# Kernel optimization log

Measured on AMD Instinct MI355X. Metric: run time of the kernel, lower is better.

## Reference

```python
import jax, jax.numpy as jnp
from jax import lax
import numpy as np

B, H, W = 8, 256, 256
NH = 128          # num_hiddens
NRH = 32          # num_residual_hiddens
K = 1024          # num_embeddings
D = 128           # embedding_dim
CC = 0.25         # commitment_cost


def setup_inputs() -> dict:
    key = jax.random.key(0)
    ks = jax.random.split(key, 18)

    def w(k, shape):
        fan_in = int(np.prod(shape[1:]))
        return (jax.random.normal(k, shape, jnp.float32) / np.sqrt(fan_in)).astype(jnp.float32)

    inp = {
        "x": jax.random.normal(ks[0], (B, 3, H, W), jnp.float32),
        # encoder
        "enc_c1": w(ks[1], (NH // 2, 3, 4, 4)),        # conv4x4 s2
        "enc_c2": w(ks[2], (NH, NH // 2, 4, 4)),       # conv4x4 s2
        "enc_c3": w(ks[3], (NH, NH, 3, 3)),            # conv3x3
        "enc_r1a": w(ks[4], (NRH, NH, 3, 3)),
        "enc_r1b": w(ks[5], (NH, NRH, 1, 1)),
        "enc_r2a": w(ks[6], (NRH, NH, 3, 3)),
        "enc_r2b": w(ks[7], (NH, NRH, 1, 1)),
        "pre_vq_w": w(ks[8], (D, NH, 1, 1)),
        # codebook: uniform(-1/K, 1/K) as in original init
        "codebook": jax.random.uniform(ks[9], (K, D), jnp.float32, -1.0 / K, 1.0 / K),
        # decoder
        "dec_c1": w(ks[10], (NH, D, 3, 3)),
        "dec_r1a": w(ks[11], (NRH, NH, 3, 3)),
        "dec_r1b": w(ks[12], (NH, NRH, 1, 1)),
        "dec_r2a": w(ks[13], (NRH, NH, 3, 3)),
        "dec_r2b": w(ks[14], (NH, NRH, 1, 1)),
        # ConvTranspose2d weight, torch layout [Cin, Cout, 4, 4]
        "dec_dc": w(ks[15], (NH, NH // 2, 4, 4)),
        "dec_c3": w(ks[16], (3, NH // 2, 3, 3)),
    }
    return inp


def _conv(x, w, s, p):
    return lax.conv_general_dilated(x, w, (s, s), ((p, p), (p, p)),
                                    dimension_numbers=("NCHW", "OIHW", "NCHW"))


def _deconv4x4_s2_p1(x, w_t):
    # torch ConvTranspose2d(k=4, s=2, p=1): flip kernel, swap in/out, lhs-dilate
    w = jnp.transpose(w_t[:, :, ::-1, ::-1], (1, 0, 2, 3))  # [Cout, Cin, 4, 4]
    return lax.conv_general_dilated(x, w, (1, 1), ((2, 2), (2, 2)),
                                    lhs_dilation=(2, 2),
                                    dimension_numbers=("NCHW", "OIHW", "NCHW"))


def _res_stack(x, r1a, r1b, r2a, r2b):
    for a, b in ((r1a, r1b), (r2a, r2b)):
        h = _conv(jax.nn.relu(x), a, 1, 1)
        h = _conv(jax.nn.relu(h), b, 1, 0)
        x = x + h
    return jax.nn.relu(x)


def _resize1d_align(x, axis, out_size):
    n = x.shape[axis]
    pos = jnp.arange(out_size, dtype=jnp.float32) * ((n - 1) / (out_size - 1))
    lo = jnp.floor(pos).astype(jnp.int32)
    hi = jnp.minimum(lo + 1, n - 1)
    wt = (pos - lo.astype(jnp.float32)).astype(x.dtype)
    shape = [1] * x.ndim
    shape[axis] = out_size
    wt = wt.reshape(shape)
    return jnp.take(x, lo, axis=axis) * (1 - wt) + jnp.take(x, hi, axis=axis) * wt


def _upsample2x_bilinear_align(x):  # align_corners=True, separable
    x = _resize1d_align(x, 2, 2 * x.shape[2])
    return _resize1d_align(x, 3, 2 * x.shape[3])


def reference(x, enc_c1, enc_c2, enc_c3, enc_r1a, enc_r1b, enc_r2a, enc_r2b,
              pre_vq_w, codebook, dec_c1, dec_r1a, dec_r1b, dec_r2a, dec_r2b,
              dec_dc, dec_c3):
    # ---- encoder ----
    h = jax.nn.relu(_conv(x, enc_c1, 2, 1))
    h = jax.nn.relu(_conv(h, enc_c2, 2, 1))
    h = _conv(h, enc_c3, 1, 1)            # note: no relu here (matches source)
    h = _res_stack(h, enc_r1a, enc_r1b, enc_r2a, enc_r2b)
    z = _conv(h, pre_vq_w, 1, 0)          # [B, D, H/4, W/4]

    # ---- VQ (eval mode: no EMA update, q_latent_loss = 0) ----
    zp = jnp.transpose(z, (0, 2, 3, 1))               # [B, h, w, D]
    flat = zp.reshape(-1, D)                          # [N, D]
    dist = (jnp.sum(flat * flat, axis=1, keepdims=True)
            + jnp.sum(codebook * codebook, axis=1)
            - 2.0 * flat @ codebook.T)                # [N, K]
    idx = jnp.argmin(dist, axis=1)                    # [N]
    q = codebook[idx].reshape(zp.shape)               # gather lookup
    e_latent_loss = jnp.mean((lax.stop_gradient(q) - zp) ** 2)
    loss = CC * e_latent_loss
    q_st = zp + lax.stop_gradient(q - zp)             # straight-through
    counts = jnp.zeros((K,), jnp.float32).at[idx].add(1.0)
    avg_probs = counts / flat.shape[0]
    perplexity = jnp.exp(-jnp.sum(avg_probs * jnp.log(avg_probs + 1e-10)))
    quantized = jnp.transpose(q_st, (0, 3, 1, 2))     # [B, D, h, w]

    # ---- decoder ----
    d = _conv(quantized, dec_c1, 1, 1)
    d = _res_stack(d, dec_r1a, dec_r1b, dec_r2a, dec_r2b)
    d = jax.nn.relu(_deconv4x4_s2_p1(d, dec_dc))
    d = _upsample2x_bilinear_align(d)
    d = _conv(d, dec_c3, 1, 1)
    recon = 2.0 * jax.nn.sigmoid(d) - 1.0             # [B, 3, H, W]
    return loss, recon, perplexity
```

## Files before the change

kernel.cpp:

```cpp
#include <hip/hip_runtime.h>
#include <hip/hip_bf16.h>
#include <math.h>

#define CC_COST 0.25

typedef __attribute__((ext_vector_type(8))) short short8v;
typedef __attribute__((ext_vector_type(4))) float f32x4;
typedef __attribute__((ext_vector_type(16))) float f32x16;

__device__ __forceinline__ unsigned short f2bf(float f) {
    unsigned u = __float_as_uint(f);
    unsigned r = (u + 0x7FFFu + ((u >> 16) & 1u)) >> 16;
    return (unsigned short)r;
}
__device__ __forceinline__ float bf2f(unsigned short h) {
    return __uint_as_float(((unsigned)h) << 16);
}


struct WtJobs {
    const float* src[15];
    float* dst[15];
    int cout[15], cin[15], kk[15], kind[15];
    int blk0[16];
};

__global__ void wt_batch_k(WtJobs J)
{
    int blk = blockIdx.x;
    int j = 0;
    while (j < 14 && blk >= J.blk0[j + 1]) ++j;
    int i = (blk - J.blk0[j]) * 256 + threadIdx.x;
    int total = J.cout[j] * J.cin[j] * J.kk[j];
    if (i >= total) return;
    const float* src = J.src[j];
    float* dst = J.dst[j];
    int kind = J.kind[j];
    if (kind == 0) {
        int Cout = J.cout[j], Cin = J.cin[j], KK = J.kk[j];
        int oc = i % Cout; int t2 = i / Cout; int t = t2 % KK; int c = t2 / KK;
        dst[i] = src[(oc * Cin + c) * KK + t];
    } else {
        int o = i % 3; int t = (i / 3) % 9; int c = i / 27;
        dst[i] = src[(o * 64 + c) * 9 + t];
    }
}

__global__ void wt_split_k(const float* __restrict__ w,
                           unsigned short* __restrict__ whi,
                           unsigned short* __restrict__ wlo)
{
    int i = blockIdx.x * 256 + threadIdx.x;
    if (i >= 147456) return;
    int ci = i & 15;
    int oc = (i >> 4) & 127;
    int rest = i >> 11;
    int cb = rest & 7;
    int tap = rest >> 3;
    float v = w[(oc * 128 + cb * 16 + ci) * 9 + tap];
    unsigned short h = f2bf(v);
    whi[i] = h;
    wlo[i] = f2bf(v - bf2f(h));
}

__global__ void wt_split4_k(const float* __restrict__ w,
                            unsigned short* __restrict__ whi,
                            unsigned short* __restrict__ wlo)
{
    int i = blockIdx.x * 256 + threadIdx.x;
    if (i >= 131072) return;
    int t = i & 15;
    int oc = (i >> 4) & 127;
    int rest = i >> 11;
    int cb = rest & 3;
    int tap = rest >> 2;
    float v = w[(oc * 64 + cb * 16 + t) * 16 + tap];
    unsigned short h = f2bf(v);
    whi[i] = h;
    wlo[i] = f2bf(v - bf2f(h));
}

__global__ void wt_split_dc_k(const float* __restrict__ w,
                              unsigned short* __restrict__ whi,
                              unsigned short* __restrict__ wlo)
{
    int i = blockIdx.x * 256 + threadIdx.x;
    if (i >= 131072) return;
    int ci = i & 15;
    int oc = (i >> 4) & 63;
    int cb = (i >> 10) & 7;
    int kx = (i >> 13) & 3;
    int ky = i >> 15;
    float v = w[((size_t)(cb * 16 + ci) * 64 + oc) * 16 + ky * 4 + kx];
    unsigned short h = f2bf(v);
    whi[i] = h;
    wlo[i] = f2bf(v - bf2f(h));
}

__global__ void wt_split_r_k(const float* __restrict__ w,
                             unsigned short* __restrict__ whi,
                             unsigned short* __restrict__ wlo)
{
    int i = blockIdx.x * 256 + threadIdx.x;
    if (i >= 36864) return;
    int k5 = i & 31;
    int oc = (i >> 5) & 31;
    int cb = (i >> 10) & 3;
    int tap = i >> 12;
    float v = w[(oc * 128 + cb * 32 + k5) * 9 + tap];
    unsigned short h = f2bf(v);
    whi[i] = h;
    wlo[i] = f2bf(v - bf2f(h));
}

__global__ void wt_split_1x1_k(const float* __restrict__ w,
                               unsigned short* __restrict__ whi,
                               unsigned short* __restrict__ wlo)
{
    int i = blockIdx.x * 256 + threadIdx.x;
    if (i >= 4096) return;
    int ci = i & 15;
    int oc = (i >> 4) & 127;
    int kk = i >> 11;
    float v = w[oc * 32 + kk * 16 + ci];
    unsigned short h = f2bf(v);
    whi[i] = h;
    wlo[i] = f2bf(v - bf2f(h));
}

__global__ void wt_split_up_k(const float* __restrict__ w,
                              unsigned short* __restrict__ whi,
                              unsigned short* __restrict__ wlo)
{
    int i = blockIdx.x * 256 + threadIdx.x;
    if (i >= 18432) return;
    int ci = i & 15;
    int oc = (i >> 4) & 31;
    int cb = (i >> 9) & 3;
    int tap = i >> 11;
    float v = 0.f;
    if (oc < 3) {
        int ch = cb * 16 + ci;
        v = w[(oc * 64 + ch) * 9 + tap];
    }
    unsigned short h = f2bf(v);
    whi[i] = h;
    wlo[i] = f2bf(v - bf2f(h));
}

__global__ __launch_bounds__(512) void conv3x3_mfma(
    const float* __restrict__ in,
    const unsigned short* __restrict__ whi,
    const unsigned short* __restrict__ wlo,
    float* __restrict__ out)
{
    constexpr int CST = 40;
    __shared__ unsigned short ls_hi[4 * 68 * CST];
    __shared__ unsigned short ls_lo[4 * 68 * CST];

    int tid = threadIdx.x;
    int lane = tid & 63;
    int w = tid >> 6;
    int myrow = w & 1;
    int oc0 = (w >> 1) * 32;
    int y0 = (blockIdx.x & 31) * 2;
    int b  = blockIdx.x >> 5;
    int ln31 = lane & 31;
    int lhf  = lane >> 5;

    f32x16 acc0 = {};
    f32x16 acc1 = {};

    const float* inb = in + (size_t)b * 128 * 4096;

    for (int chunk = 0; chunk < 4; ++chunk) {
        int c0 = chunk * 32;
        __syncthreads();
        for (int i = tid; i < 4 * 66 * 16; i += 512) {
            int x = i % 66;
            int t = i / 66;
            int cp = t & 15;
            int r = t >> 4;
            int gy = y0 - 1 + r, gx = x - 1;
            float v0 = 0.f, v1 = 0.f;
            if ((unsigned)gy < 64u && (unsigned)gx < 64u) {
                const float* p = inb + (size_t)(c0 + 2 * cp) * 4096 + gy * 64 + gx;
                v0 = p[0];
                v1 = p[4096];
            }
            unsigned short h0 = f2bf(v0), h1 = f2bf(v1);
            unsigned short l0 = f2bf(v0 - bf2f(h0)), l1 = f2bf(v1 - bf2f(h1));
            int a = (r * 68 + x) * CST + 2 * cp;
            *reinterpret_cast<unsigned int*>(&ls_hi[a]) = (unsigned)h0 | ((unsigned)h1 << 16);
            *reinterpret_cast<unsigned int*>(&ls_lo[a]) = (unsigned)l0 | ((unsigned)l1 << 16);
        }
        __syncthreads();

        #pragma unroll
        for (int tap = 0; tap < 9; ++tap) {
            int dy = tap / 3, dx = tap - 3 * (tap / 3);
            int rbase = (myrow + dy) * 68;
            #pragma unroll
            for (int cb = 0; cb < 2; ++cb) {
                int cbg = chunk * 2 + cb;
                size_t wofs = (((size_t)tap * 8 + cbg) * 128 + oc0 + ln31) * 16 + lhf * 8;
                short8v ah = *reinterpret_cast<const short8v*>(whi + wofs);
                short8v al = *reinterpret_cast<const short8v*>(wlo + wofs);
                int k0 = cb * 16 + lhf * 8;
                int xo0 = (rbase + ln31 + dx) * CST + k0;
                int xo1 = (rbase + 32 + ln31 + dx) * CST + k0;
                short8v bh0 = *reinterpret_cast<const short8v*>(&ls_hi[xo0]);
                short8v bl0 = *reinterpret_cast<const short8v*>(&ls_lo[xo0]);
                short8v bh1 = *reinterpret_cast<const short8v*>(&ls_hi[xo1]);
                short8v bl1 = *reinterpret_cast<const short8v*>(&ls_lo[xo1]);
                acc0 = __builtin_amdgcn_mfma_f32_32x32x16_bf16(ah, bh0, acc0, 0, 0, 0);
                acc1 = __builtin_amdgcn_mfma_f32_32x32x16_bf16(ah, bh1, acc1, 0, 0, 0);
                acc0 = __builtin_amdgcn_mfma_f32_32x32x16_bf16(ah, bl0, acc0, 0, 0, 0);
                acc1 = __builtin_amdgcn_mfma_f32_32x32x16_bf16(ah, bl1, acc1, 0, 0, 0);
                acc0 = __builtin_amdgcn_mfma_f32_32x32x16_bf16(al, bh0, acc0, 0, 0, 0);
                acc1 = __builtin_amdgcn_mfma_f32_32x32x16_bf16(al, bh1, acc1, 0, 0, 0);
            }
        }
    }

    float* ob = out + (size_t)b * 128 * 4096 + (size_t)(y0 + myrow) * 64;
    #pragma unroll
    for (int r = 0; r < 16; ++r) {
        int oc = oc0 + (r & 3) + 8 * (r >> 2) + 4 * lhf;
        ob[(size_t)oc * 4096 + ln31]      = acc0[r];
        ob[(size_t)oc * 4096 + 32 + ln31] = acc1[r];
    }
}

__global__ __launch_bounds__(512) void conv4x4s2_mfma(
    const float* __restrict__ in,
    const unsigned short* __restrict__ whi,
    const unsigned short* __restrict__ wlo,
    float* __restrict__ out)
{
    constexpr int CST = 24;
    __shared__ unsigned short lsEh[6 * 65 * CST];
    __shared__ unsigned short lsEl[6 * 65 * CST];
    __shared__ unsigned short lsOh[6 * 65 * CST];
    __shared__ unsigned short lsOl[6 * 65 * CST];

    int tid = threadIdx.x;
    int lane = tid & 63;
    int w = tid >> 6;
    int myrow = w & 1;
    int oc0 = (w >> 1) * 32;
    int y0 = (blockIdx.x & 31) * 2;
    int b  = blockIdx.x >> 5;
    int ln31 = lane & 31;
    int lhf  = lane >> 5;

    f32x16 acc0 = {};
    f32x16 acc1 = {};

    const float* inb = in + (size_t)b * 64 * 16384;

    for (int cb = 0; cb < 4; ++cb) {
        int c0 = cb * 16;
        __syncthreads();
        for (int i = tid; i < 12480; i += 512) {
            int gxi = i % 130; int t2 = i / 130;
            int r = t2 % 6; int cc = t2 / 6;
            int gx = gxi - 1;
            int gy = 2 * y0 - 1 + r;
            float v = 0.f;
            if ((unsigned)gy < 128u && (unsigned)gx < 128u)
                v = inb[(size_t)(c0 + cc) * 16384 + gy * 128 + gx];
            unsigned short h = f2bf(v);
            unsigned short l = f2bf(v - bf2f(h));
            if (gx & 1) {
                int a = (r * 65 + ((gx + 1) >> 1)) * CST + cc;
                lsOh[a] = h; lsOl[a] = l;
            } else {
                int a = (r * 65 + (gx >> 1)) * CST + cc;
                lsEh[a] = h; lsEl[a] = l;
            }
        }
        __syncthreads();

        #pragma unroll
        for (int tap = 0; tap < 16; ++tap) {
            int ky = tap >> 2, kx = tap & 3;
            int ridx = 2 * myrow + ky;
            int dlt = kx >> 1;
            const unsigned short* ph = (kx & 1) ? lsEh : lsOh;
            const unsigned short* pl = (kx & 1) ? lsEl : lsOl;
            size_t aoff = ((size_t)((tap * 4 + cb) * 128 + oc0 + ln31)) * 16 + lhf * 8;
            short8v ah = *reinterpret_cast<const short8v*>(whi + aoff);
            short8v al = *reinterpret_cast<const short8v*>(wlo + aoff);
            int base0 = (ridx * 65 + ln31 + dlt) * CST + lhf * 8;
            int base1 = (ridx * 65 + 32 + ln31 + dlt) * CST + lhf * 8;
            short8v bh0 = *reinterpret_cast<const short8v*>(ph + base0);
            short8v bl0 = *reinterpret_cast<const short8v*>(pl + base0);
            short8v bh1 = *reinterpret_cast<const short8v*>(ph + base1);
            short8v bl1 = *reinterpret_cast<const short8v*>(pl + base1);
            acc0 = __builtin_amdgcn_mfma_f32_32x32x16_bf16(ah, bh0, acc0, 0, 0, 0);
            acc1 = __builtin_amdgcn_mfma_f32_32x32x16_bf16(ah, bh1, acc1, 0, 0, 0);
            acc0 = __builtin_amdgcn_mfma_f32_32x32x16_bf16(ah, bl0, acc0, 0, 0, 0);
            acc1 = __builtin_amdgcn_mfma_f32_32x32x16_bf16(ah, bl1, acc1, 0, 0, 0);
            acc0 = __builtin_amdgcn_mfma_f32_32x32x16_bf16(al, bh0, acc0, 0, 0, 0);
            acc1 = __builtin_amdgcn_mfma_f32_32x32x16_bf16(al, bh1, acc1, 0, 0, 0);
        }
    }

    int y = y0 + myrow;
    float* ob = out + (size_t)b * 128 * 4096 + (size_t)y * 64;
    #pragma unroll
    for (int r = 0; r < 16; ++r) {
        int oc = oc0 + (r & 3) + 8 * (r >> 2) + 4 * lhf;
        ob[(size_t)oc * 4096 + ln31]      = fmaxf(acc0[r], 0.f);
        ob[(size_t)oc * 4096 + 32 + ln31] = fmaxf(acc1[r], 0.f);
    }
}

__global__ __launch_bounds__(512) void deconv_mfma(
    const float* __restrict__ in,
    const unsigned short* __restrict__ whi,
    const unsigned short* __restrict__ wlo,
    float* __restrict__ out)
{
    constexpr int CST = 40;
    __shared__ unsigned short ls_hi[3 * 68 * CST];
    __shared__ unsigned short ls_lo[3 * 68 * CST];

    int tid = threadIdx.x;
    int lane = tid & 63;
    int w = tid >> 6;
    int myrow = w & 1;
    int oc0 = ((w >> 1) & 1) * 32;
    int oxp = w >> 2;
    int yb = blockIdx.x & 63;
    int b  = blockIdx.x >> 6;
    int ln31 = lane & 31;
    int lhf  = lane >> 5;

    f32x16 acc0 = {};
    f32x16 acc1 = {};

    const float* inb = in + (size_t)b * 128 * 4096;

    for (int chunk = 0; chunk < 4; ++chunk) {
        int c0 = chunk * 32;
        __syncthreads();
        for (int i = tid; i < 3 * 66 * 16; i += 512) {
            int x = i % 66;
            int t = i / 66;
            int cp = t & 15;
            int r = t >> 4;
            int gy = yb - 1 + r, gx = x - 1;
            float v0 = 0.f, v1 = 0.f;
            if ((unsigned)gy < 64u && (unsigned)gx < 64u) {
                const float* p = inb + (size_t)(c0 + 2 * cp) * 4096 + gy * 64 + gx;
                v0 = fmaxf(p[0], 0.f);
                v1 = fmaxf(p[4096], 0.f);
            }
            unsigned short h0 = f2bf(v0), h1 = f2bf(v1);
            unsigned short l0 = f2bf(v0 - bf2f(h0)), l1 = f2bf(v1 - bf2f(h1));
            int a = (r * 68 + x) * CST + 2 * cp;
            *reinterpret_cast<unsigned int*>(&ls_hi[a]) = (unsigned)h0 | ((unsigned)h1 << 16);
            *reinterpret_cast<unsigned int*>(&ls_lo[a]) = (unsigned)l0 | ((unsigned)l1 << 16);
        }
        __syncthreads();

        #pragma unroll
        for (int tki = 0; tki < 2; ++tki) {
            int ky = (1 - myrow) + 2 * tki;
            int ldsrow = 1 + myrow - tki;
            #pragma unroll
            for (int txi = 0; txi < 2; ++txi) {
                int kx = (1 - oxp) + 2 * txi;
                int dlt = oxp - txi;
                #pragma unroll
                for (int cb = 0; cb < 2; ++cb) {
                    int cbg = chunk * 2 + cb;
                    size_t aoff = ((size_t)(((ky * 4 + kx) * 8 + cbg) * 64 + oc0 + ln31)) * 16 + lhf * 8;
                    short8v ah = *reinterpret_cast<const short8v*>(whi + aoff);
                    short8v al = *reinterpret_cast<const short8v*>(wlo + aoff);
                    int k0 = cb * 16 + lhf * 8;
                    int xo0 = (ldsrow * 68 + ln31 + dlt + 1) * CST + k0;
                    int xo1 = (ldsrow * 68 + 32 + ln31 + dlt + 1) * CST + k0;
                    short8v bh0 = *reinterpret_cast<const short8v*>(&ls_hi[xo0]);
                    short8v bl0 = *reinterpret_cast<const short8v*>(&ls_lo[xo0]);
                    short8v bh1 = *reinterpret_cast<const short8v*>(&ls_hi[xo1]);
                    short8v bl1 = *reinterpret_cast<const short8v*>(&ls_lo[xo1]);
                    acc0 = __builtin_amdgcn_mfma_f32_32x32x16_bf16(ah, bh0, acc0, 0, 0, 0);
                    acc1 = __builtin_amdgcn_mfma_f32_32x32x16_bf16(ah, bh1, acc1, 0, 0, 0);
                    acc0 = __builtin_amdgcn_mfma_f32_32x32x16_bf16(ah, bl0, acc0, 0, 0, 0);
                    acc1 = __builtin_amdgcn_mfma_f32_32x32x16_bf16(ah, bl1, acc1, 0, 0, 0);
                    acc0 = __builtin_amdgcn_mfma_f32_32x32x16_bf16(al, bh0, acc0, 0, 0, 0);
                    acc1 = __builtin_amdgcn_mfma_f32_32x32x16_bf16(al, bh1, acc1, 0, 0, 0);
                }
            }
        }
    }

    int oy = 2 * yb + myrow;
    float* ob = out + (size_t)b * 64 * 16384 + (size_t)oy * 128;
    #pragma unroll
    for (int r = 0; r < 16; ++r) {
        int oc = oc0 + (r & 3) + 8 * (r >> 2) + 4 * lhf;
        ob[(size_t)oc * 16384 + oxp + 2 * ln31]      = fmaxf(acc0[r], 0.f);
        ob[(size_t)oc * 16384 + oxp + 64 + 2 * ln31] = fmaxf(acc1[r], 0.f);
    }
}

__global__ __launch_bounds__(512) void fused_res_k(
    const float* __restrict__ in,
    const unsigned short* __restrict__ whi,
    const unsigned short* __restrict__ wlo,
    const unsigned short* __restrict__ w1hi,
    const unsigned short* __restrict__ w1lo,
    float* __restrict__ out)
{
    constexpr int CST = 40;
    __shared__ unsigned short ls_hi[3 * 68 * CST];
    __shared__ unsigned short ls_lo[3 * 68 * CST];

    int tid = threadIdx.x;
    int lane = tid & 63;
    int w = tid >> 6;
    int oc0 = (w & 1) * 16;
    int px0 = (w >> 1) * 16;
    int y = blockIdx.x & 63;
    int b = blockIdx.x >> 6;
    int n16 = lane & 15;
    int kk4 = lane >> 4;
    int ln31 = lane & 31;
    int lhf = lane >> 5;

    f32x4 acc = {};
    const float* inb = in + (size_t)b * 128 * 4096;

    for (int cb = 0; cb < 4; ++cb) {
        int c0 = cb * 32;
        __syncthreads();
        for (int i = tid; i < 3 * 66 * 16; i += 512) {
            int x = i % 66;
            int t = i / 66;
            int cp = t & 15;
            int r = t >> 4;
            int gy = y - 1 + r, gx = x - 1;
            float v0 = 0.f, v1 = 0.f;
            if ((unsigned)gy < 64u && (unsigned)gx < 64u) {
                const float* p = inb + (size_t)(c0 + 2 * cp) * 4096 + gy * 64 + gx;
                v0 = fmaxf(p[0], 0.f);
                v1 = fmaxf(p[4096], 0.f);
            }
            unsigned short h0 = f2bf(v0), h1 = f2bf(v1);
            unsigned short l0 = f2bf(v0 - bf2f(h0)), l1 = f2bf(v1 - bf2f(h1));
            int a = (r * 68 + x) * CST + 2 * cp;
            *reinterpret_cast<unsigned int*>(&ls_hi[a]) = (unsigned)h0 | ((unsigned)h1 << 16);
            *reinterpret_cast<unsigned int*>(&ls_lo[a]) = (unsigned)l0 | ((unsigned)l1 << 16);
        }
        __syncthreads();

        #pragma unroll
        for (int tap = 0; tap < 9; ++tap) {
            int dy = tap / 3, dx = tap - 3 * (tap / 3);
            size_t aoff = ((size_t)((tap * 4 + cb) * 32 + oc0 + n16)) * 32 + kk4 * 8;
            short8v ah = *reinterpret_cast<const short8v*>(whi + aoff);
            short8v al = *reinterpret_cast<const short8v*>(wlo + aoff);
            int xo = (dy * 68 + px0 + n16 + dx) * CST + kk4 * 8;
            short8v bh = *reinterpret_cast<const short8v*>(&ls_hi[xo]);
            short8v bl = *reinterpret_cast<const short8v*>(&ls_lo[xo]);
            acc = __builtin_amdgcn_mfma_f32_16x16x32_bf16(ah, bh, acc, 0, 0, 0);
            acc = __builtin_amdgcn_mfma_f32_16x16x32_bf16(ah, bl, acc, 0, 0, 0);
            acc = __builtin_amdgcn_mfma_f32_16x16x32_bf16(al, bh, acc, 0, 0, 0);
        }
    }

    __syncthreads();
    #pragma unroll
    for (int r = 0; r < 4; ++r) {
        int ch = oc0 + kk4 * 4 + r;
        int px = px0 + n16;
        float v = fmaxf(acc[r], 0.f);
        unsigned short h = f2bf(v);
        ls_hi[px * CST + ch] = h;
        ls_lo[px * CST + ch] = f2bf(v - bf2f(h));
    }
    __syncthreads();

    int oc1 = (w & 3) * 32;
    int pxt = (w >> 2) * 32;
    f32x16 acc2 = {};
    #pragma unroll
    for (int kk = 0; kk < 2; ++kk) {
        size_t aoff = ((size_t)(kk * 128 + oc1 + ln31)) * 16 + lhf * 8;
        short8v ah = *reinterpret_cast<const short8v*>(w1hi + aoff);
        short8v al = *reinterpret_cast<const short8v*>(w1lo + aoff);
        int boff = (pxt + ln31) * CST + kk * 16 + lhf * 8;
        short8v bh = *reinterpret_cast<const short8v*>(&ls_hi[boff]);
        short8v bl = *reinterpret_cast<const short8v*>(&ls_lo[boff]);
        acc2 = __builtin_amdgcn_mfma_f32_32x32x16_bf16(ah, bh, acc2, 0, 0, 0);
        acc2 = __builtin_amdgcn_mfma_f32_32x32x16_bf16(ah, bl, acc2, 0, 0, 0);
        acc2 = __builtin_amdgcn_mfma_f32_32x32x16_bf16(al, bh, acc2, 0, 0, 0);
    }

    float* ob = out + (size_t)b * 128 * 4096 + (size_t)y * 64;
    const float* rb = inb + (size_t)y * 64;
    #pragma unroll
    for (int r = 0; r < 16; ++r) {
        int oc = oc1 + (r & 3) + 8 * (r >> 2) + 4 * lhf;
        size_t o = (size_t)oc * 4096 + pxt + ln31;
        ob[o] = rb[o] + acc2[r];
    }
}

template<int CIN, int COUT, int CC, bool IN_RELU, bool ADD_RES>
__global__ __launch_bounds__(256) void conv1x1_k(
    const float* __restrict__ in, const float* __restrict__ wT,
    const float* __restrict__ res, float* __restrict__ out)
{
    static_assert(COUT == 128, "tile assumes 128");
    __shared__ __align__(16) float ls_in[CC][64];
    __shared__ __align__(16) float ls_w[CC][COUT];
    int tid = threadIdx.x;
    int pxg = tid & 7, ocg = tid >> 3;
    int x0 = pxg * 8, oc0 = ocg * 4;
    int y = blockIdx.x & 63, b = blockIdx.x >> 6;

    float acc[4][8];
    #pragma unroll
    for (int o = 0; o < 4; ++o)
        #pragma unroll
        for (int p = 0; p < 8; ++p) acc[o][p] = 0.f;

    for (int c0 = 0; c0 < CIN; c0 += CC) {
        __syncthreads();
        for (int i = tid; i < CC * 64; i += 256) {
            int xx = i & 63, cc = i >> 6;
            float v = in[(((size_t)b * CIN + c0 + cc) * 64 + y) * 64 + xx];
            if (IN_RELU) v = fmaxf(v, 0.f);
            ls_in[cc][xx] = v;
        }
        const float* wsrc = wT + (size_t)c0 * COUT;
        for (int i = tid; i < CC * COUT; i += 256)
            (&ls_w[0][0])[i] = wsrc[i];
        __syncthreads();

        for (int cc = 0; cc < CC; ++cc) {
            float rv[8];
            const float* base = &ls_in[cc][x0];
            float4 v0 = *reinterpret_cast<const float4*>(base);
            float4 v1 = *reinterpret_cast<const float4*>(base + 4);
            rv[0]=v0.x; rv[1]=v0.y; rv[2]=v0.z; rv[3]=v0.w;
            rv[4]=v1.x; rv[5]=v1.y; rv[6]=v1.z; rv[7]=v1.w;
            float4 w4 = *reinterpret_cast<const float4*>(&ls_w[cc][oc0]);
            float wv[4] = {w4.x, w4.y, w4.z, w4.w};
            #pragma unroll
            for (int p = 0; p < 8; ++p)
                #pragma unroll
                for (int o = 0; o < 4; ++o)
                    acc[o][p] = fmaf(rv[p], wv[o], acc[o][p]);
        }
    }
    #pragma unroll
    for (int o = 0; o < 4; ++o) {
        float* op = out + (((size_t)b * COUT + oc0 + o) * 64 + y) * 64 + x0;
        const float* rp = res + (((size_t)b * COUT + oc0 + o) * 64 + y) * 64 + x0;
        #pragma unroll
        for (int q = 0; q < 2; ++q) {
            float4 v = make_float4(acc[o][4*q], acc[o][4*q+1],
                                   acc[o][4*q+2], acc[o][4*q+3]);
            if (ADD_RES) {
                float4 r4 = *reinterpret_cast<const float4*>(rp + 4 * q);
                v.x += r4.x; v.y += r4.y; v.z += r4.z; v.w += r4.w;
            }
            *reinterpret_cast<float4*>(op + 4 * q) = v;
        }
    }
}

template<int CIN, int COUT, int WOUT, int CC, int OCB, int WOC, int NSLICE>
__global__ __launch_bounds__(256) void conv4x4s2_k(
    const float* __restrict__ in, const float* __restrict__ wT,
    float* __restrict__ out)
{
    constexpr int WIN = WOUT * 2;
    constexpr int NPXG = WOUT / 8, NOCG = COUT / OCB;
    static_assert(NPXG * NOCG == 256, "bad tile");
    constexpr int WUSE = 2 * WOUT + 2;
    constexpr int PADLEN = ((WUSE + (WUSE / 16 + 1) * 4) + 3) & ~3;
    __shared__ __align__(16) float ls_in[CC][4][PADLEN];
    __shared__ __align__(16) float ls_w[CC][16][COUT];

    int tid = threadIdx.x;
    int pxg = tid % NPXG, ocg = tid / NPXG;
    int x0 = pxg * 8, oc0 = ocg * OCB;
    int blk = blockIdx.x;
    int y = blk % WOUT; int rest = blk / WOUT;
    int slice = rest % NSLICE; int b = rest / NSLICE;
    int oc_base = slice * COUT;
    const float* inb = in + (size_t)b * CIN * WIN * WIN;

    float acc[OCB][8];
    #pragma unroll
    for (int o = 0; o < OCB; ++o)
        #pragma unroll
        for (int p = 0; p < 8; ++p) acc[o][p] = 0.f;

    for (int c0 = 0; c0 < CIN; c0 += CC) {
        __syncthreads();
        for (int i = tid; i < CC * 4 * WUSE; i += 256) {
            int xx = i % WUSE; int t = i / WUSE; int r = t & 3; int cc = t >> 2;
            int gy = 2 * y - 1 + r, gx = xx - 1;
            float v = 0.f;
            if ((unsigned)gy < (unsigned)WIN && (unsigned)gx < (unsigned)WIN)
                v = inb[(c0 + cc) * WIN * WIN + gy * WIN + gx];
            ls_in[cc][r][xx + ((xx >> 4) << 2)] = v;
        }
        const float* wsrc = wT + (size_t)c0 * 16 * WOC + oc_base;
        for (int i = tid; i < CC * 16 * COUT; i += 256) {
            int o = i % COUT; int tt = (i / COUT) % 16; int cc = i / (16 * COUT);
            ls_w[cc][tt][o] = wsrc[(cc * 16 + tt) * WOC + o];
        }
        __syncthreads();

        for (int cc = 0; cc < CC; ++cc) {
            const float* lw = &ls_w[cc][0][0];
            #pragma unroll
            for (int ky = 0; ky < 4; ++ky) {
                float rv[18];
                const float* base = &ls_in[cc][ky][20 * pxg];
                #pragma unroll
                for (int q = 0; q < 4; ++q) {
                    float4 v = *reinterpret_cast<const float4*>(base + 4 * q);
                    rv[4*q]=v.x; rv[4*q+1]=v.y; rv[4*q+2]=v.z; rv[4*q+3]=v.w;
                }
                rv[16] = base[20]; rv[17] = base[21];
                #pragma unroll
                for (int kx = 0; kx < 4; ++kx) {
                    const float* wp = lw + (ky * 4 + kx) * COUT + oc0;
                    float wv[OCB];
                    if constexpr (OCB == 4) {
                        float4 w4 = *reinterpret_cast<const float4*>(wp);
                        wv[0]=w4.x; wv[1]=w4.y; wv[2]=w4.z; wv[3]=w4.w;
                    } else {
                        float2 w2 = *reinterpret_cast<const float2*>(wp);
                        wv[0]=w2.x; wv[1]=w2.y;
                    }
                    #pragma unroll
                    for (int p = 0; p < 8; ++p) {
                        float iv = rv[2 * p + kx];
                        #pragma unroll
                        for (int o = 0; o < OCB; ++o)
                            acc[o][p] = fmaf(iv, wv[o], acc[o][p]);
                    }
                }
            }
        }
    }
    #pragma unroll
    for (int o = 0; o < OCB; ++o) {
        float* op = out + (((size_t)b * (COUT * NSLICE) + oc_base + oc0 + o) * WOUT + y) * WOUT + x0;
        #pragma unroll
        for (int q = 0; q < 2; ++q) {
            float4 v = make_float4(fmaxf(acc[o][4*q],0.f), fmaxf(acc[o][4*q+1],0.f),
                                   fmaxf(acc[o][4*q+2],0.f), fmaxf(acc[o][4*q+3],0.f));
            *reinterpret_cast<float4*>(op + 4 * q) = v;
        }
    }
}

__global__ __launch_bounds__(512) void upconv_mfma(
    const float* __restrict__ in,
    const unsigned short* __restrict__ whi,
    const unsigned short* __restrict__ wlo,
    float* __restrict__ out)
{
    constexpr int CST = 24;
    __shared__ unsigned short ls_hi[6 * 68 * CST];
    __shared__ unsigned short ls_lo[6 * 68 * CST];
    __shared__ float xfx[68];
    __shared__ int   xloT[68];

    int tid = threadIdx.x;
    int lane = tid & 63;
    int w = tid >> 6;
    int myrow = w & 3;
    int pt = w >> 2;
    int blk = blockIdx.x;
    int xq = blk & 3;
    int yblk = (blk >> 2) & 63;
    int b = blk >> 8;
    int xbase = xq * 64;
    int y0 = yblk * 4;
    int ln31 = lane & 31;
    int lhf = lane >> 5;
    const float SCL = 127.0f / 255.0f;
    const float* hb = in + (size_t)b * 64 * 16384;

    if (tid < 68) {
        int ux = xbase - 1 + tid;
        bool v = ((unsigned)ux < 256u);
        float px = (v ? ux : 0) * SCL;
        int lo = (int)px;
        xloT[tid] = lo;
        xfx[tid] = v ? (px - (float)lo) : -1.0f;
    }

    f32x16 acc = {};

    for (int chunk = 0; chunk < 4; ++chunk) {
        int c0 = chunk * 16;
        __syncthreads();
        for (int i = tid; i < 6 * 68 * 8; i += 512) {
            int xx = i % 68; int t = i / 68; int cp = t & 7; int r = t >> 3;
            int uy = y0 - 1 + r;
            float v0 = 0.f, v1 = 0.f;
            float fx = xfx[xx];
            if ((unsigned)uy < 256u && fx >= 0.f) {
                float py = uy * SCL;
                int ylo = (int)py; int yhi = min(ylo + 1, 127);
                float fy = py - (float)ylo;
                int lo = xloT[xx]; int hi = min(lo + 1, 127);
                const float* hp = hb + (size_t)(c0 + 2 * cp) * 16384;
                const float* p0 = hp + ylo * 128;
                const float* p1 = hp + yhi * 128;
                float a = p0[lo], b2 = p0[hi], c2 = p1[lo], d2 = p1[hi];
                float top = a + (b2 - a) * fx;
                float bot = c2 + (d2 - c2) * fx;
                v0 = top + (bot - top) * fy;
                const float* q0 = p0 + 16384;
                const float* q1 = p1 + 16384;
                float a2 = q0[lo], b3 = q0[hi], c3 = q1[lo], d3 = q1[hi];
                float top2 = a2 + (b3 - a2) * fx;
                float bot2 = c3 + (d3 - c3) * fx;
                v1 = top2 + (bot2 - top2) * fy;
            }
            unsigned short h0 = f2bf(v0), h1 = f2bf(v1);
            unsigned short l0 = f2bf(v0 - bf2f(h0)), l1 = f2bf(v1 - bf2f(h1));
            int a = (r * 68 + xx) * CST + 2 * cp;
            *reinterpret_cast<unsigned int*>(&ls_hi[a]) = (unsigned)h0 | ((unsigned)h1 << 16);
            *reinterpret_cast<unsigned int*>(&ls_lo[a]) = (unsigned)l0 | ((unsigned)l1 << 16);
        }
        __syncthreads();

        #pragma unroll
        for (int tap = 0; tap < 9; ++tap) {
            int dy = tap / 3, dx = tap - 3 * (tap / 3);
            size_t aoff = ((size_t)((tap * 4 + chunk) * 32 + ln31)) * 16 + lhf * 8;
            short8v ah = *reinterpret_cast<const short8v*>(whi + aoff);
            short8v al = *reinterpret_cast<const short8v*>(wlo + aoff);
            int boff = ((myrow + dy) * 68 + pt * 32 + ln31 + dx) * CST + lhf * 8;
            short8v bh = *reinterpret_cast<const short8v*>(&ls_hi[boff]);
            short8v bl = *reinterpret_cast<const short8v*>(&ls_lo[boff]);
            acc = __builtin_amdgcn_mfma_f32_32x32x16_bf16(ah, bh, acc, 0, 0, 0);
            acc = __builtin_amdgcn_mfma_f32_32x32x16_bf16(ah, bl, acc, 0, 0, 0);
            acc = __builtin_amdgcn_mfma_f32_32x32x16_bf16(al, bh, acc, 0, 0, 0);
        }
    }

    if (lhf == 0) {
        int y = y0 + myrow;
        int x0 = xbase + pt * 32 + ln31;
        #pragma unroll
        for (int r = 0; r < 3; ++r) {
            float v = 2.f / (1.f + expf(-acc[r])) - 1.f;
            out[(((size_t)b * 3 + r) * 256 + y) * 256 + x0] = v;
        }
    }
}

__global__ void prep_codebook(const float* __restrict__ cb,
                              unsigned short* __restrict__ cbh,
                              unsigned short* __restrict__ cbl,
                              float* __restrict__ ce2,
                              unsigned int* __restrict__ counts)
{
    int k = blockIdx.x * 256 + threadIdx.x;
    if (k >= 1024) return;
    float s = 0.f;
    for (int d = 0; d < 128; ++d) {
        float v = cb[k * 128 + d];
        s = fmaf(v, v, s);
        unsigned short h = f2bf(v);
        int kk = d >> 4, t = d & 15;
        cbh[(kk * 1024 + k) * 16 + t] = h;
        cbl[(kk * 1024 + k) * 16 + t] = f2bf(v - bf2f(h));
    }
    ce2[k] = s;
    counts[k] = 0u;
}

__global__ __launch_bounds__(512) void vq_fused(
    const float* __restrict__ z, const float* __restrict__ cb,
    const unsigned short* __restrict__ cbh,
    const unsigned short* __restrict__ cbl,
    const float* __restrict__ ce2,
    unsigned int* __restrict__ counts, float* __restrict__ q,
    double* __restrict__ partial)
{
    constexpr int ZP = 136;
    __shared__ unsigned short zh[64 * ZP];
    __shared__ unsigned short zlo[64 * ZP];
    __shared__ float ce2l[1024];
    __shared__ float cmbd[4][2][32];
    __shared__ int   cmbi[4][2][32];
    __shared__ int sidx[64];
    __shared__ float red[8];

    int tid = threadIdx.x;
    int lane = tid & 63;
    int w = tid >> 6;
    int pxg = w & 1;
    int cgrp = w >> 1;
    int ln31 = lane & 31;
    int lhf = lane >> 5;
    int p0g = blockIdx.x * 64;
    int b = p0g >> 12;
    int p0 = p0g & 4095;

    for (int i = tid; i < 8192; i += 512) {
        int d = i >> 6, px = i & 63;
        float v = z[((size_t)b * 128 + d) * 4096 + p0 + px];
        unsigned short h = f2bf(v);
        zh[px * ZP + d]  = h;
        zlo[px * ZP + d] = f2bf(v - bf2f(h));
    }
    for (int i = tid; i < 1024; i += 512) ce2l[i] = ce2[i];
    __syncthreads();

    int pxrow = pxg * 32 + ln31;
    short8v zfh[8], zfl[8];
    #pragma unroll
    for (int kk = 0; kk < 8; ++kk) {
        int off = pxrow * ZP + kk * 16 + lhf * 8;
        zfh[kk] = *reinterpret_cast<const short8v*>(&zh[off]);
        zfl[kk] = *reinterpret_cast<const short8v*>(&zlo[off]);
    }

    float best = 3.4e38f; int bidx = 0;
    #pragma unroll
    for (int ct = 0; ct < 8; ++ct) {
        int c0 = cgrp * 256 + ct * 32;
        f32x16 acc = {};
        #pragma unroll
        for (int kk = 0; kk < 8; ++kk) {
            size_t aoff = ((size_t)(kk * 1024 + c0 + ln31)) * 16 + lhf * 8;
            short8v ah = *reinterpret_cast<const short8v*>(cbh + aoff);
            short8v al = *reinterpret_cast<const short8v*>(cbl + aoff);
            acc = __builtin_amdgcn_mfma_f32_32x32x16_bf16(ah, zfh[kk], acc, 0, 0, 0);
            acc = __builtin_amdgcn_mfma_f32_32x32x16_bf16(ah, zfl[kk], acc, 0, 0, 0);
            acc = __builtin_amdgcn_mfma_f32_32x32x16_bf16(al, zfh[kk], acc, 0, 0, 0);
        }
        #pragma unroll
        for (int r = 0; r < 16; ++r) {
            int code = c0 + (r & 3) + 8 * (r >> 2) + 4 * lhf;
            float dist = ce2l[code] - 2.f * acc[r];
            if (dist < best || (dist == best && code < bidx)) { best = dist; bidx = code; }
        }
    }
    {
        float ob = __shfl_xor(best, 32);
        int   oi = __shfl_xor(bidx, 32);
        if (ob < best || (ob == best && oi < bidx)) { best = ob; bidx = oi; }
    }
    if (lane < 32) { cmbd[cgrp][pxg][lane] = best; cmbi[cgrp][pxg][lane] = bidx; }
    __syncthreads();
    if (tid < 64) {
        int pg = tid >> 5, l = tid & 31;
        float bv = cmbd[0][pg][l]; int bi = cmbi[0][pg][l];
        #pragma unroll
        for (int g = 1; g < 4; ++g) {
            float ov = cmbd[g][pg][l]; int oi = cmbi[g][pg][l];
            if (ov < bv || (ov == bv && oi < bi)) { bv = ov; bi = oi; }
        }
        sidx[pg * 32 + l] = bi;
        atomicAdd(&counts[bi], 1u);
    }
    __syncthreads();

    int pix = tid & 63, dg = tid >> 6;
    int kidx = sidx[pix];
    const float* crow = cb + (size_t)kidx * 128 + dg * 16;
    float sq = 0.f;
    size_t zbase = ((size_t)b * 128 + dg * 16) * 4096 + p0 + pix;
    #pragma unroll
    for (int ii = 0; ii < 4; ++ii) {
        float4 c4 = *reinterpret_cast<const float4*>(crow + 4 * ii);
        float vals[4] = {c4.x, c4.y, c4.z, c4.w};
        #pragma unroll
        for (int jj = 0; jj < 4; ++jj) {
            int dl = ii * 4 + jj;
            float qv = vals[jj];
            float zv = z[zbase + (size_t)dl * 4096];
            float df = qv - zv;
            sq = fmaf(df, df, sq);
            q[zbase + (size_t)dl * 4096] = qv;
        }
    }
    #pragma unroll
    for (int off = 32; off > 0; off >>= 1) sq += __shfl_xor(sq, off);
    if (lane == 0) red[w] = sq;
    __syncthreads();
    if (tid == 0) {
        double s = 0.0;
        #pragma unroll
        for (int ww = 0; ww < 8; ++ww) s += (double)red[ww];
        partial[blockIdx.x] = s;
    }
}

__global__ __launch_bounds__(256) void finalize_kernel(
    const double* __restrict__ partial, const unsigned int* __restrict__ counts,
    float* __restrict__ dout)
{
    __shared__ double sd[256];
    __shared__ double lossSh;
    int tid = threadIdx.x;
    double s = 0.0;
    for (int i = tid; i < 512; i += 256) s += partial[i];
    sd[tid] = s; __syncthreads();
    for (int off = 128; off > 0; off >>= 1) {
        if (tid < off) sd[tid] += sd[tid + off];
        __syncthreads();
    }
    if (tid == 0) lossSh = CC_COST * sd[0] / 4194304.0;
    __syncthreads();

    double h = 0.0;
    for (int k = tid; k < 1024; k += 256) {
        double pp = (double)counts[k] / 32768.0;
        h += pp * log(pp + 1e-10);
    }
    sd[tid] = h; __syncthreads();
    for (int off = 128; off > 0; off >>= 1) {
        if (tid < off) sd[tid] += sd[tid + off];
        __syncthreads();
    }
    if (tid == 0) {
        dout[0]       = (float)lossSh;
        dout[1572865] = (float)exp(-sd[0]);
    }
}

extern "C" void kernel_launch(void* const* d_in, const int* in_sizes, int n_in,
                              void* d_out, int out_size, void* d_ws, size_t ws_size,
                              hipStream_t stream)
{
    const float* x        = (const float*)d_in[0];
    const float* enc_c1   = (const float*)d_in[1];
    const float* enc_c2   = (const float*)d_in[2];
    const float* enc_c3   = (const float*)d_in[3];
    const float* enc_r1a  = (const float*)d_in[4];
    const float* enc_r1b  = (const float*)d_in[5];
    const float* enc_r2a  = (const float*)d_in[6];
    const float* enc_r2b  = (const float*)d_in[7];
    const float* pre_vq_w = (const float*)d_in[8];
    const float* codebook = (const float*)d_in[9];
    const float* dec_c1   = (const float*)d_in[10];
    const float* dec_r1a  = (const float*)d_in[11];
    const float* dec_r1b  = (const float*)d_in[12];
    const float* dec_r2a  = (const float*)d_in[13];
    const float* dec_r2b  = (const float*)d_in[14];
    const float* dec_dc   = (const float*)d_in[15];
    const float* dec_c3   = (const float*)d_in[16];
    float* dout = (float*)d_out;

    char* wsp = (char*)d_ws;
    auto alloc = [&](size_t bytes) {
        void* p = (void*)wsp;
        wsp += (bytes + 255) & ~(size_t)255;
        return p;
    };
    float* h1   = (float*)alloc(8ull*64*128*128*4);
    float* bufA = (float*)alloc(8ull*128*64*64*4);
    float* bufB = (float*)alloc(8ull*128*64*64*4);
    unsigned short* cbh = (unsigned short*)alloc(131072*2);
    unsigned short* cbl = (unsigned short*)alloc(131072*2);
    float* ce2  = (float*)alloc(1024*4);
    unsigned int* counts = (unsigned int*)alloc(1024*4);
    double* partial = (double*)alloc(512*8);
    float* wt_ec1  = (float*)alloc(3072*4);
    float* wt_pvq  = (float*)alloc(16384*4);
    unsigned short* w3hi_e = (unsigned short*)alloc(147456*2);
    unsigned short* w3lo_e = (unsigned short*)alloc(147456*2);
    unsigned short* w3hi_d = (unsigned short*)alloc(147456*2);
    unsigned short* w3lo_d = (unsigned short*)alloc(147456*2);
    unsigned short* w4hi   = (unsigned short*)alloc(131072*2);
    unsigned short* w4lo   = (unsigned short*)alloc(131072*2);
    unsigned short* wdchi  = (unsigned short*)alloc(131072*2);
    unsigned short* wdclo  = (unsigned short*)alloc(131072*2);
    unsigned short* wr1aeh = (unsigned short*)alloc(36864*2);
    unsigned short* wr1ael = (unsigned short*)alloc(36864*2);
    unsigned short* wr2aeh = (unsigned short*)alloc(36864*2);
    unsigned short* wr2ael = (unsigned short*)alloc(36864*2);
    unsigned short* wr1adh = (unsigned short*)alloc(36864*2);
    unsigned short* wr1adl = (unsigned short*)alloc(36864*2);
    unsigned short* wr2adh = (unsigned short*)alloc(36864*2);
    unsigned short* wr2adl = (unsigned short*)alloc(36864*2);
    unsigned short* w1e1h  = (unsigned short*)alloc(4096*2);
    unsigned short* w1e1l  = (unsigned short*)alloc(4096*2);
    unsigned short* w1e2h  = (unsigned short*)alloc(4096*2);
    unsigned short* w1e2l  = (unsigned short*)alloc(4096*2);
    unsigned short* w1d1h  = (unsigned short*)alloc(4096*2);
    unsigned short* w1d1l  = (unsigned short*)alloc(4096*2);
    unsigned short* w1d2h  = (unsigned short*)alloc(4096*2);
    unsigned short* w1d2l  = (unsigned short*)alloc(4096*2);
    unsigned short* wuph   = (unsigned short*)alloc(18432*2);
    unsigned short* wupl   = (unsigned short*)alloc(18432*2);
    float* zb = bufA;
    float* qb = h1;

    prep_codebook<<<4, 256, 0, stream>>>(codebook, cbh, cbl, ce2, counts);

    WtJobs J;
    const float* srcs[2] = {enc_c1, pre_vq_w};
    float* dsts[2] = {wt_ec1, wt_pvq};
    int couts[2] = {64, 128};
    int cins[2]  = {3, 128};
    int kks[2]   = {16, 1};
    int kinds[2] = {0, 0};
    int off = 0;
    for (int j = 0; j < 2; ++j) {
        J.src[j] = srcs[j]; J.dst[j] = dsts[j];
        J.cout[j] = couts[j]; J.cin[j] = cins[j]; J.kk[j] = kks[j];
        J.kind[j] = kinds[j];
        J.blk0[j] = off;
        off += (couts[j] * cins[j] * kks[j] + 255) / 256;
    }
    J.blk0[2] = off;
    for (int j = 3; j < 16; ++j) J.blk0[j] = off + 1000000;
    wt_batch_k<<<off, 256, 0, stream>>>(J);
    wt_split_k<<<576, 256, 0, stream>>>(enc_c3, w3hi_e, w3lo_e);
    wt_split_k<<<576, 256, 0, stream>>>(dec_c1, w3hi_d, w3lo_d);
    wt_split4_k<<<512, 256, 0, stream>>>(enc_c2, w4hi, w4lo);
    wt_split_dc_k<<<512, 256, 0, stream>>>(dec_dc, wdchi, wdclo);
    wt_split_r_k<<<144, 256, 0, stream>>>(enc_r1a, wr1aeh, wr1ael);
    wt_split_r_k<<<144, 256, 0, stream>>>(enc_r2a, wr2aeh, wr2ael);
    wt_split_r_k<<<144, 256, 0, stream>>>(dec_r1a, wr1adh, wr1adl);
    wt_split_r_k<<<144, 256, 0, stream>>>(dec_r2a, wr2adh, wr2adl);
    wt_split_1x1_k<<<16, 256, 0, stream>>>(enc_r1b, w1e1h, w1e1l);
    wt_split_1x1_k<<<16, 256, 0, stream>>>(enc_r2b, w1e2h, w1e2l);
    wt_split_1x1_k<<<16, 256, 0, stream>>>(dec_r1b, w1d1h, w1d1l);
    wt_split_1x1_k<<<16, 256, 0, stream>>>(dec_r2b, w1d2h, w1d2l);
    wt_split_up_k<<<72, 256, 0, stream>>>(dec_c3, wuph, wupl);

    conv4x4s2_k<3, 64, 128, 3, 4, 64, 1><<<1024, 256, 0, stream>>>(x, wt_ec1, h1);
    conv4x4s2_mfma<<<256, 512, 0, stream>>>(h1, w4hi, w4lo, bufA);
    conv3x3_mfma<<<256, 512, 0, stream>>>(bufA, w3hi_e, w3lo_e, bufB);
    fused_res_k<<<512, 512, 0, stream>>>(bufB, wr1aeh, wr1ael, w1e1h, w1e1l, bufA);
    fused_res_k<<<512, 512, 0, stream>>>(bufA, wr2aeh, wr2ael, w1e2h, w1e2l, bufB);
    conv1x1_k<128, 128, 32, true, false><<<512, 256, 0, stream>>>(bufB, wt_pvq, bufB, zb);

    vq_fused<<<512, 512, 0, stream>>>(zb, codebook, cbh, cbl, ce2, counts, qb, partial);

    conv3x3_mfma<<<256, 512, 0, stream>>>(qb, w3hi_d, w3lo_d, bufA);
    fused_res_k<<<512, 512, 0, stream>>>(bufA, wr1adh, wr1adl, w1d1h, w1d1l, bufB);
    fused_res_k<<<512, 512, 0, stream>>>(bufB, wr2adh, wr2adl, w1d2h, w1d2l, bufA);
    deconv_mfma<<<512, 512, 0, stream>>>(bufA, wdchi, wdclo, h1);
    upconv_mfma<<<2048, 512, 0, stream>>>(h1, wuph, wupl, dout + 1);

    finalize_kernel<<<1, 256, 0, stream>>>(partial, counts, dout);
}
```

Baseline: 730.6 us.

## Restructure VQ distance loop with LDS-resident z fragments and software-pipelined codebook loads

Stores the bf16 hi/lo z tiles in LDS already laid out in MFMA fragment order, so each step reads them straight from LDS instead of keeping 16 short8 vectors in registers. The codebook-tile loop is flattened into 64 steps with a four-deep prefetch of codebook loads. Two accumulators alternate so the argmin reduction of one tile can overlap the MFMAs of the next. The launch bound now requests 4 waves per SIMD to raise occupancy, at the cost of extra LDS reads per MFMA and possible register pressure from the prefetch buffers.

After: 726.7 us. Within noise of the previous version (-0.5%).

```diff
diff --git a/kernel.cpp b/kernel.cpp
--- a/kernel.cpp
+++ b/kernel.cpp
@@ -788,7 +788,7 @@
     counts[k] = 0u;
 }
 
-__global__ __launch_bounds__(512) void vq_fused(
+__global__ __launch_bounds__(512, 4) void vq_fused(
     const float* __restrict__ z, const float* __restrict__ cb,
     const unsigned short* __restrict__ cbh,
     const unsigned short* __restrict__ cbl,
@@ -796,9 +796,8 @@
     unsigned int* __restrict__ counts, float* __restrict__ q,
     double* __restrict__ partial)
 {
-    constexpr int ZP = 136;
-    __shared__ unsigned short zh[64 * ZP];
-    __shared__ unsigned short zlo[64 * ZP];
+    __shared__ unsigned short zfh_l[2][8][64][8];
+    __shared__ unsigned short zfl_l[2][8][64][8];
     __shared__ float ce2l[1024];
     __shared__ float cmbd[4][2][32];
     __shared__ int   cmbi[4][2][32];
@@ -820,42 +819,68 @@
         int d = i >> 6, px = i & 63;
         float v = z[((size_t)b * 128 + d) * 4096 + p0 + px];
         unsigned short h = f2bf(v);
-        zh[px * ZP + d]  = h;
-        zlo[px * ZP + d] = f2bf(v - bf2f(h));
+        int kk = d >> 4;
+        int lhf2 = (d >> 3) & 1;
+        int j = d & 7;
+        int lane2 = lhf2 * 32 + (px & 31);
+        int pxg2 = px >> 5;
+        zfh_l[pxg2][kk][lane2][j] = h;
+        zfl_l[pxg2][kk][lane2][j] = f2bf(v - bf2f(h));
     }
     for (int i = tid; i < 1024; i += 512) ce2l[i] = ce2[i];
     __syncthreads();
 
-    int pxrow = pxg * 32 + ln31;
-    short8v zfh[8], zfl[8];
-    #pragma unroll
-    for (int kk = 0; kk < 8; ++kk) {
-        int off = pxrow * ZP + kk * 16 + lhf * 8;
-        zfh[kk] = *reinterpret_cast<const short8v*>(&zh[off]);
-        zfl[kk] = *reinterpret_cast<const short8v*>(&zlo[off]);
-    }
+    const unsigned short* zhb = &zfh_l[pxg][0][lane][0];
+    const unsigned short* zlb = &zfl_l[pxg][0][lane][0];
 
     float best = 3.4e38f; int bidx = 0;
-    #pragma unroll
-    for (int ct = 0; ct < 8; ++ct) {
-        int c0 = cgrp * 256 + ct * 32;
-        f32x16 acc = {};
-        #pragma unroll
-        for (int kk = 0; kk < 8; ++kk) {
-            size_t aoff = ((size_t)(kk * 1024 + c0 + ln31)) * 16 + lhf * 8;
-            short8v ah = *reinterpret_cast<const short8v*>(cbh + aoff);
-            short8v al = *reinterpret_cast<const short8v*>(cbl + aoff);
-            acc = __builtin_amdgcn_mfma_f32_32x32x16_bf16(ah, zfh[kk], acc, 0, 0, 0);
-            acc = __builtin_amdgcn_mfma_f32_32x32x16_bf16(ah, zfl[kk], acc, 0, 0, 0);
-            acc = __builtin_amdgcn_mfma_f32_32x32x16_bf16(al, zfh[kk], acc, 0, 0, 0);
-        }
-        #pragma unroll
-        for (int r = 0; r < 16; ++r) {
-            int code = c0 + (r & 3) + 8 * (r >> 2) + 4 * lhf;
-            float dist = ce2l[code] - 2.f * acc[r];
-            if (dist < best || (dist == best && code < bidx)) { best = dist; bidx = code; }
-        }
-    }
+    f32x16 accA = {};
+    f32x16 accB = {};
+
+#define VQLD(S, H, L) { \
+    int ct_ = (S) >> 3, kk_ = (S) & 7; \
+    size_t ao_ = ((size_t)(kk_ * 1024 + cgrp * 256 + ct_ * 32 + ln31)) * 16 + lhf * 8; \
+    H = *reinterpret_cast<const short8v*>(cbh + ao_); \
+    L = *reinterpret_cast<const short8v*>(cbl + ao_); }
+
+#define VQRED(AC, CT) { \
+    int c0_ = cgrp * 256 + (CT) * 32; \
+    _Pragma("unroll") \
+    for (int r = 0; r < 16; ++r) { \
+        int code = c0_ + (r & 3) + 8 * (r >> 2) + 4 * lhf; \
+        float dist = ce2l[code] - 2.f * AC[r]; \
+        if (dist < best || (dist == best && code < bidx)) { best = dist; bidx = code; } \
+    } }
+
+#define VQSTEP(S, H, L) { \
+    int kk_ = (S) & 7; \
+    short8v bh_ = *reinterpret_cast<const short8v*>(zhb + kk_ * 512); \
+    short8v bl_ = *reinterpret_cast<const short8v*>(zlb + kk_ * 512); \
+    if ((((S) >> 3) & 1) == 0) { \
+        accA = __builtin_amdgcn_mfma_f32_32x32x16_bf16(H, bh_, accA, 0, 0, 0); \
+        accA = __builtin_amdgcn_mfma_f32_32x32x16_bf16(H, bl_, accA, 0, 0, 0); \
+        accA = __builtin_amdgcn_mfma_f32_32x32x16_bf16(L, bh_, accA, 0, 0, 0); \
+        if (kk_ == 7) { VQRED(accA, (S) >> 3); accA = (f32x16){}; } \
+    } else { \
+        accB = __builtin_amdgcn_mfma_f32_32x32x16_bf16(H, bh_, accB, 0, 0, 0); \
+        accB = __builtin_amdgcn_mfma_f32_32x32x16_bf16(H, bl_, accB, 0, 0, 0); \
+        accB = __builtin_amdgcn_mfma_f32_32x32x16_bf16(L, bh_, accB, 0, 0, 0); \
+        if (kk_ == 7) { VQRED(accB, (S) >> 3); accB = (f32x16){}; } \
+    } }
+
+    short8v h0, l0, h1, l1, h2, l2, h3, l3;
+    VQLD(0, h0, l0); VQLD(1, h1, l1); VQLD(2, h2, l2); VQLD(3, h3, l3);
+    #pragma unroll
+    for (int s = 0; s < 64; s += 4) {
+        { short8v A = h0, B = l0; if (s + 4 < 64) VQLD(s + 4, h0, l0); VQSTEP(s,     A, B); }
+        { short8v A = h1, B = l1; if (s + 5 < 64) VQLD(s + 5, h1, l1); VQSTEP(s + 1, A, B); }
+        { short8v A = h2, B = l2; if (s + 6 < 64) VQLD(s + 6, h2, l2); VQSTEP(s + 2, A, B); }
+        { short8v A = h3, B = l3; if (s + 7 < 64) VQLD(s + 7, h3, l3); VQSTEP(s + 3, A, B); }
+    }
+#undef VQSTEP
+#undef VQRED
+#undef VQLD
+
     {
         float ob = __shfl_xor(best, 32);
         int   oi = __shfl_xor(bidx, 32);
```

## Reuse codebook fragments across both pixel halves in VQ distance kernel

Applied to the files above, without the earlier changes.

Each wave now handles both 32-pixel groups for a 128-code slice, instead of one pixel group for a 256-code slice. Each codebook fragment loaded from global memory is therefore used by two MFMA chains, which halves codebook traffic per block. The z fragments are stored in shared memory in MFMA-lane order and read per kk step rather than held in registers. The cross-wave argmin merge now spans 8 waves. The changes add LDS reads in the inner loop, and the two accumulators raise register pressure.

Measured after the change: 724.3 us. About the same (-0.9%).

```diff
diff --git a/kernel.cpp b/kernel.cpp
--- a/kernel.cpp
+++ b/kernel.cpp
@@ -796,20 +796,17 @@
     unsigned int* __restrict__ counts, float* __restrict__ q,
     double* __restrict__ partial)
 {
-    constexpr int ZP = 136;
-    __shared__ unsigned short zh[64 * ZP];
-    __shared__ unsigned short zlo[64 * ZP];
+    __shared__ unsigned short zfh_l[2][8][64][8];
+    __shared__ unsigned short zfl_l[2][8][64][8];
     __shared__ float ce2l[1024];
-    __shared__ float cmbd[4][2][32];
-    __shared__ int   cmbi[4][2][32];
+    __shared__ float cmbd[8][64];
+    __shared__ int   cmbi[8][64];
     __shared__ int sidx[64];
     __shared__ float red[8];
 
     int tid = threadIdx.x;
     int lane = tid & 63;
     int w = tid >> 6;
-    int pxg = w & 1;
-    int cgrp = w >> 1;
     int ln31 = lane & 31;
     int lhf = lane >> 5;
     int p0g = blockIdx.x * 64;
@@ -820,58 +817,77 @@
         int d = i >> 6, px = i & 63;
         float v = z[((size_t)b * 128 + d) * 4096 + p0 + px];
         unsigned short h = f2bf(v);
-        zh[px * ZP + d]  = h;
-        zlo[px * ZP + d] = f2bf(v - bf2f(h));
+        int kk = d >> 4;
+        int lhf2 = (d >> 3) & 1;
+        int j = d & 7;
+        int lane2 = lhf2 * 32 + (px & 31);
+        int pxg2 = px >> 5;
+        zfh_l[pxg2][kk][lane2][j] = h;
+        zfl_l[pxg2][kk][lane2][j] = f2bf(v - bf2f(h));
     }
     for (int i = tid; i < 1024; i += 512) ce2l[i] = ce2[i];
     __syncthreads();
 
-    int pxrow = pxg * 32 + ln31;
-    short8v zfh[8], zfl[8];
-    #pragma unroll
-    for (int kk = 0; kk < 8; ++kk) {
-        int off = pxrow * ZP + kk * 16 + lhf * 8;
-        zfh[kk] = *reinterpret_cast<const short8v*>(&zh[off]);
-        zfl[kk] = *reinterpret_cast<const short8v*>(&zlo[off]);
-    }
-
-    float best = 3.4e38f; int bidx = 0;
-    #pragma unroll
-    for (int ct = 0; ct < 8; ++ct) {
-        int c0 = cgrp * 256 + ct * 32;
-        f32x16 acc = {};
+    const unsigned short* zh0 = &zfh_l[0][0][lane][0];
+    const unsigned short* zl0 = &zfl_l[0][0][lane][0];
+    const unsigned short* zh1 = &zfh_l[1][0][lane][0];
+    const unsigned short* zl1 = &zfl_l[1][0][lane][0];
+
+    float best0 = 3.4e38f, best1 = 3.4e38f;
+    int bidx0 = 0, bidx1 = 0;
+
+    for (int ct = 0; ct < 4; ++ct) {
+        int c0 = w * 128 + ct * 32;
+        f32x16 acc0 = {};
+        f32x16 acc1 = {};
         #pragma unroll
         for (int kk = 0; kk < 8; ++kk) {
-            size_t aoff = ((size_t)(kk * 1024 + c0 + ln31)) * 16 + lhf * 8;
-            short8v ah = *reinterpret_cast<const short8v*>(cbh + aoff);
-            short8v al = *reinterpret_cast<const short8v*>(cbl + aoff);
-            acc = __builtin_amdgcn_mfma_f32_32x32x16_bf16(ah, zfh[kk], acc, 0, 0, 0);
-            acc = __builtin_amdgcn_mfma_f32_32x32x16_bf16(ah, zfl[kk], acc, 0, 0, 0);
-            acc = __builtin_amdgcn_mfma_f32_32x32x16_bf16(al, zfh[kk], acc, 0, 0, 0);
+            size_t ao = ((size_t)(kk * 1024 + c0 + ln31)) * 16 + lhf * 8;
+            short8v ah = *reinterpret_cast<const short8v*>(cbh + ao);
+            short8v al = *reinterpret_cast<const short8v*>(cbl + ao);
+            short8v bh0 = *reinterpret_cast<const short8v*>(zh0 + kk * 512);
+            short8v bl0 = *reinterpret_cast<const short8v*>(zl0 + kk * 512);
+            short8v bh1 = *reinterpret_cast<const short8v*>(zh1 + kk * 512);
+            short8v bl1 = *reinterpret_cast<const short8v*>(zl1 + kk * 512);
+            acc0 = __builtin_amdgcn_mfma_f32_32x32x16_bf16(ah, bh0, acc0, 0, 0, 0);
+            acc1 = __builtin_amdgcn_mfma_f32_32x32x16_bf16(ah, bh1, acc1, 0, 0, 0);
+            acc0 = __builtin_amdgcn_mfma_f32_32x32x16_bf16(ah, bl0, acc0, 0, 0, 0);
+            acc1 = __builtin_amdgcn_mfma_f32_32x32x16_bf16(ah, bl1, acc1, 0, 0, 0);
+            acc0 = __builtin_amdgcn_mfma_f32_32x32x16_bf16(al, bh0, acc0, 0, 0, 0);
+            acc1 = __builtin_amdgcn_mfma_f32_32x32x16_bf16(al, bh1, acc1, 0, 0, 0);
         }
         #pragma unroll
         for (int r = 0; r < 16; ++r) {
             int code = c0 + (r & 3) + 8 * (r >> 2) + 4 * lhf;
-            float dist = ce2l[code] - 2.f * acc[r];
-            if (dist < best || (dist == best && code < bidx)) { best = dist; bidx = code; }
-        }
-    }
+            float ce = ce2l[code];
+            float d0 = ce - 2.f * acc0[r];
+            float d1 = ce - 2.f * acc1[r];
+            if (d0 < best0 || (d0 == best0 && code < bidx0)) { best0 = d0; bidx0 = code; }
+            if (d1 < best1 || (d1 == best1 && code < bidx1)) { best1 = d1; bidx1 = code; }
+        }
+    }
+
     {
-        float ob = __shfl_xor(best, 32);
-        int   oi = __shfl_xor(bidx, 32);
-        if (ob < best || (ob == best && oi < bidx)) { best = ob; bidx = oi; }
-    }
-    if (lane < 32) { cmbd[cgrp][pxg][lane] = best; cmbi[cgrp][pxg][lane] = bidx; }
+        float ob = __shfl_xor(best0, 32);
+        int   oi = __shfl_xor(bidx0, 32);
+        if (ob < best0 || (ob == best0 && oi < bidx0)) { best0 = ob; bidx0 = oi; }
+        ob = __shfl_xor(best1, 32);
+        oi = __shfl_xor(bidx1, 32);
+        if (ob < best1 || (ob == best1 && oi < bidx1)) { best1 = ob; bidx1 = oi; }
+    }
+    if (lane < 32) {
+        cmbd[w][ln31] = best0;      cmbi[w][ln31] = bidx0;
+        cmbd[w][32 + ln31] = best1; cmbi[w][32 + ln31] = bidx1;
+    }
     __syncthreads();
     if (tid < 64) {
-        int pg = tid >> 5, l = tid & 31;
-        float bv = cmbd[0][pg][l]; int bi = cmbi[0][pg][l];
-        #pragma unroll
-        for (int g = 1; g < 4; ++g) {
-            float ov = cmbd[g][pg][l]; int oi = cmbi[g][pg][l];
+        float bv = cmbd[0][tid]; int bi = cmbi[0][tid];
+        #pragma unroll
+        for (int g = 1; g < 8; ++g) {
+            float ov = cmbd[g][tid]; int oi = cmbi[g][tid];
             if (ov < bv || (ov == bv && oi < bi)) { bv = ov; bi = oi; }
         }
-        sidx[pg * 32 + l] = bi;
+        sidx[tid] = bi;
         atomicAdd(&counts[bi], 1u);
     }
     __syncthreads();
```
